# Optimization experiments

Measured on AMD Instinct MI355X. Metric: run time of the kernel, lower is better.

The kernel has to match this reference:

```python
import jax, jax.numpy as jnp
import numpy as np


def _conv2d(x, w, b):
    # 3x3 conv, stride 1, pad 1, NCHW
    y = jax.lax.conv_general_dilated(x, w, (1, 1), ((1, 1), (1, 1)),
                                     dimension_numbers=('NCHW', 'OIHW', 'NCHW'))
    return y + b[None, :, None, None]


def _up2(x):
    return jnp.repeat(jnp.repeat(x, 2, axis=2), 2, axis=3)


def _mdconv(x, w, b, ow, ob):
    # Modulated deformable conv v2 (mmcv semantics): 3x3, stride 1, pad 1,
    # dilation 1, deformable_groups=1. Offsets/mask predicted by conv_offset,
    # out = chunk3 -> (o1, o2, mask); offset = cat(o1, o2); mask = sigmoid(mask).
    B, Cin, H, W = x.shape
    off = _conv2d(x, ow, ob)                        # [B,27,H,W]
    o1, o2, m = jnp.split(off, 3, axis=1)
    offs = jnp.concatenate([o1, o2], axis=1)        # [B,18,H,W]
    dy, dx = offs[:, 0::2], offs[:, 1::2]           # [B,9,H,W] (dy,dx interleaved per kernel pt)
    mask = jax.nn.sigmoid(m)                        # [B,9,H,W]
    ky, kx = jnp.meshgrid(jnp.arange(3), jnp.arange(3), indexing='ij')
    # sampling positions: p0 + pn + offset (pad=1)
    py = jnp.arange(H, dtype=x.dtype)[None, None, :, None] - 1.0 + ky.reshape(1, 9, 1, 1) + dy
    px = jnp.arange(W, dtype=x.dtype)[None, None, None, :] - 1.0 + kx.reshape(1, 9, 1, 1) + dx
    y0 = jnp.floor(py); x0 = jnp.floor(px)
    wy1 = py - y0; wx1 = px - x0
    y0i = y0.astype(jnp.int32); x0i = x0.astype(jnp.int32)
    flat = x.reshape(B, Cin, H * W)

    def gather(yi, xi):
        valid = ((yi >= 0) & (yi < H) & (xi >= 0) & (xi < W)).astype(x.dtype)  # zero padding
        idx = jnp.clip(yi, 0, H - 1) * W + jnp.clip(xi, 0, W - 1)             # [B,9,H,W]
        g = jax.vmap(lambda f, i: f[:, i])(flat, idx)                          # [B,Cin,9,H,W]
        return g * valid[:, None]

    val = (gather(y0i, x0i) * ((1 - wy1) * (1 - wx1))[:, None]
           + gather(y0i, x0i + 1) * ((1 - wy1) * wx1)[:, None]
           + gather(y0i + 1, x0i) * (wy1 * (1 - wx1))[:, None]
           + gather(y0i + 1, x0i + 1) * (wy1 * wx1)[:, None])
    cols = val * mask[:, None]                      # [B,Cin,9,H,W]
    out = jnp.einsum('ock,bckhw->bohw', w.reshape(w.shape[0], Cin, 9), cols)
    return out + b[None, :, None, None]


def setup_inputs() -> dict:
    key = jax.random.key(0)
    ks = jax.random.split(key, 24)
    C = 256
    sizes = [(96, 96), (48, 48), (24, 24), (12, 12)]
    d = {}
    for i, (h, w) in enumerate(sizes):
        d[f'x{i}'] = jax.random.normal(ks[i], (2, C, h, w), dtype=jnp.float32)
    for i in range(4):
        d[f'w{i}'] = jax.random.normal(ks[4 + i], (C, C, 3, 3), dtype=jnp.float32) * 0.02
        d[f'b{i}'] = jax.random.normal(ks[8 + i], (C,), dtype=jnp.float32) * 0.02
    for i in range(1, 4):
        d[f'ow{i}'] = jax.random.normal(ks[12 + i], (27, C, 3, 3), dtype=jnp.float32) * 0.01
        d[f'ob{i}'] = jax.random.normal(ks[16 + i], (27,), dtype=jnp.float32) * 0.01
    return d


def reference(x0, x1, x2, x3, w0, w1, w2, w3, b0, b1, b2, b3,
              ow1, ow2, ow3, ob1, ob2, ob3):
    # tdm_convs[3] called with level=1 -> deform; the same-size nearest interpolate is identity
    t3 = _mdconv(x3, w3, b3, ow3, ob3)
    # i=3: tdm_convs[2](2, x2 + up(t3)) -> deform
    t2 = _mdconv(x2 + _up2(t3), w2, b2, ow2, ob2)
    # i=2: tdm_convs[1](1, x1 + up(t2)) -> deform
    t1 = _mdconv(x1 + _up2(t2), w1, b1, ow1, ob1)
    # i=1: tdm_convs[0](0, x0 + up(t1)) -> level 0 < start_level -> plain conv
    t0 = _conv2d(x0 + _up2(t1), w0, b0)
    return (t0, t1, t2, t3)
```

## Files before the change

### kernel.cpp

```cpp
#include <hip/hip_runtime.h>
#include <math.h>

__device__ __forceinline__ ushort f2bf(float f) {
    unsigned int u = __float_as_uint(f);
    u += 0x7FFFu + ((u >> 16) & 1u);
    return (ushort)(u >> 16);
}

typedef __attribute__((address_space(1))) const unsigned int guint;
typedef __attribute__((address_space(3))) unsigned int luint;
__device__ __forceinline__ void gload_lds16(const void* g, void* l) {
    __builtin_amdgcn_global_load_lds((guint*)g, (luint*)l, 16, 0, 0);
}

using bfrag = __attribute__((ext_vector_type(8))) short;
using f4    = __attribute__((ext_vector_type(4))) float;

__device__ __forceinline__ void bf8_to_f(uint4 v, float* o) {
    unsigned int u[4] = {v.x, v.y, v.z, v.w};
    #pragma unroll
    for (int i = 0; i < 4; ++i) {
        o[2 * i]     = __uint_as_float(u[i] << 16);
        o[2 * i + 1] = __uint_as_float(u[i] & 0xFFFF0000u);
    }
}

struct CvtArgs {
    const float* src[7];
    ushort*      dst[7];
    int          m[7];
};
__global__ __launch_bounds__(256) void cvt_kernel(CvtArgs a) {
    int t = blockIdx.y;
    int idx = blockIdx.x * 256 + threadIdx.x;
    int M = a.m[t];
    if (idx >= M * 288) return;
    int m = idx / 288, rem = idx - m * 288;
    int r = rem >> 5, c8 = rem & 31;
    const float* s = a.src[t] + ((size_t)(m * 256 + c8 * 8)) * 9 + r;
    ushort vals[8];
    #pragma unroll
    for (int j = 0; j < 8; ++j) vals[j] = f2bf(s[j * 9]);
    *(uint4*)&a.dst[t][(size_t)m * 2304 + r * 256 + c8 * 8] = *(uint4*)vals;
}

struct FillArgs {
    float* outp[3];
    const float* bias[3];
    int HW[3];
    float* zbase;
    int z4;
};
__global__ __launch_bounds__(256) void fill_kernel(FillArgs a) {
    int y = blockIdx.y;
    int i = blockIdx.x * 256 + threadIdx.x;
    if (y < 3) {
        int HW = a.HW[y];
        int total4 = (2 * 256 * HW) >> 2;
        if (i < total4) {
            int e = i << 2;
            int m = (e / HW) & 255;
            float v = a.bias[y][m];
            *(float4*)&a.outp[y][e] = float4{v, v, v, v};
        }
    } else {
        if (i < a.z4) ((float4*)a.zbase)[i] = float4{0.f, 0.f, 0.f, 0.f};
    }
}

__global__ __launch_bounds__(256) void xs_nhwc(
    const float* __restrict__ x, const float* __restrict__ prev,
    ushort* __restrict__ xs, int H, int W)
{
    __shared__ ushort tile[32][72];
    const int HW = H * W, W2 = W >> 1;
    int b = blockIdx.z, c0 = blockIdx.y * 32, hw0 = blockIdx.x * 64;
    const float* xb = x + ((size_t)b * 256 + c0) * HW;
    const float* pb = prev ? prev + ((size_t)b * 256 + c0) * (HW >> 2) : nullptr;

    int hwl = threadIdx.x & 63, cl0 = threadIdx.x >> 6;
    int hw = hw0 + hwl;
    bool ok = hw < HW;
    int hwc = ok ? hw : HW - 1;
    int h = hwc / W, w = hwc - h * W;
    int pidx = (h >> 1) * W2 + (w >> 1);
    #pragma unroll
    for (int p = 0; p < 8; ++p) {
        int cl = p * 4 + cl0;
        float v = 0.f;
        if (ok) {
            v = xb[(size_t)cl * HW + hw];
            if (pb) v += pb[(size_t)cl * (HW >> 2) + pidx];
        }
        tile[cl][hwl] = f2bf(v);
    }
    __syncthreads();
    int hwl2 = threadIdx.x >> 2, cc = (threadIdx.x & 3) * 8;
    int hw2 = hw0 + hwl2;
    if (hw2 < HW) {
        ushort vals[8];
        #pragma unroll
        for (int j = 0; j < 8; ++j) vals[j] = tile[cc + j][hwl2];
        *(uint4*)&xs[((size_t)b * HW + hw2) * 256 + c0 + cc] = *(uint4*)vals;
    }
}

__global__ __launch_bounds__(256) void off_mfma(
    const ushort* __restrict__ A, const ushort* __restrict__ xs,
    const ushort* __restrict__ zeros, float* __restrict__ offbuf,
    int N, int H, int W, int ktiles)
{
    __shared__ __align__(16) ushort As[2][32 * 32];
    __shared__ __align__(16) ushort Bs[2][64 * 32];
    const int b  = blockIdx.z;
    const int n0 = blockIdx.x * 64;
    const int kt0 = blockIdx.y * ktiles * 32;
    const int tid = threadIdx.x, lane = tid & 63, wv = tid >> 6;
    const ushort* xb = xs + (size_t)b * N * 256;

    int n = n0 + (tid >> 2); if (n >= N) n = N - 1;
    int h = n / W, w = n - h * W;
    int kcc = (tid & 3) * 8;

    auto stage = [&](int kt, int bi) {
        int r = kt >> 8, c0k = kt & 255;
        int ry = r / 3 - 1, rx = r - (r / 3) * 3 - 1;
        if (tid < 128) {
            int row = tid >> 2; if (row > 26) row = 26;
            gload_lds16(A + (size_t)row * 2304 + kt + kcc,
                        (char*)As[bi] + (size_t)(tid & ~63) * 16);
        }
        int ih = h + ry, iw = w + rx;
        const ushort* src = (ih >= 0 && ih < H && iw >= 0 && iw < W)
            ? xb + (((size_t)(ih * W + iw)) << 8) + c0k + kcc
            : zeros;
        gload_lds16(src, (char*)Bs[bi] + (size_t)(tid & ~63) * 16);
    };

    f4 acc[2] = {};
    stage(kt0, 0);
    for (int kk = 0; kk < ktiles; ++kk) {
        __syncthreads();
        if (kk + 1 < ktiles) stage(kt0 + (kk + 1) * 32, (kk + 1) & 1);
        const ushort* as = As[kk & 1];
        const ushort* bs = Bs[kk & 1];
        bfrag bf = *(const bfrag*)&bs[(wv * 16 + (lane & 15)) * 32 + (lane >> 4) * 8];
        bfrag a0 = *(const bfrag*)&as[(lane & 15) * 32 + (lane >> 4) * 8];
        bfrag a1 = *(const bfrag*)&as[(16 + (lane & 15)) * 32 + (lane >> 4) * 8];
        acc[0] = __builtin_amdgcn_mfma_f32_16x16x32_bf16(a0, bf, acc[0], 0, 0, 0);
        acc[1] = __builtin_amdgcn_mfma_f32_16x16x32_bf16(a1, bf, acc[1], 0, 0, 0);
    }

    int nn = n0 + wv * 16 + (lane & 15);
    if (nn < N) {
        #pragma unroll
        for (int mb = 0; mb < 2; ++mb)
            #pragma unroll
            for (int t = 0; t < 4; ++t) {
                int m = mb * 16 + (lane >> 4) * 4 + t;
                if (m < 27)
                    atomicAdd(&offbuf[((size_t)b * 27 + m) * N + nn], acc[mb][t]);
            }
    }
}

__global__ __launch_bounds__(256) void sampling_kernel(
    const ushort* __restrict__ xs, const float* __restrict__ off,
    const float* __restrict__ ob, ushort* __restrict__ cols,
    int H, int W)
{
    __shared__ float4 gw[32][9];
    __shared__ int4   go[32][9];
    const int HW = H * W;
    const int b = blockIdx.z;
    const int hw0 = blockIdx.x * 32;
    const int tid = threadIdx.x;
    const float* offb = off + (size_t)b * 27 * HW;
    const ushort* xb = xs + (size_t)b * HW * 256;

    for (int it = tid; it < 32 * 9; it += 256) {
        int hwl = it / 9, k = it - hwl * 9;
        int hw = hw0 + hwl; if (hw >= HW) hw = HW - 1;
        int h = hw / W, w = hw - h * W;
        float dy = offb[(size_t)(2 * k) * HW + hw] + ob[2 * k];
        float dx = offb[(size_t)(2 * k + 1) * HW + hw] + ob[2 * k + 1];
        float mv = offb[(size_t)(18 + k) * HW + hw] + ob[18 + k];
        float mk = 1.0f / (1.0f + __expf(-mv));
        float py = (float)h - 1.0f + (float)(k / 3) + dy;
        float px = (float)w - 1.0f + (float)(k % 3) + dx;
        float y0f = floorf(py), x0f = floorf(px);
        float wy = py - y0f, wx = px - x0f;
        int y0 = (int)y0f, x0i = (int)x0f;
        int y1 = y0 + 1, x1 = x0i + 1;
        bool vy0 = (y0 >= 0) & (y0 < H), vy1 = (y1 >= 0) & (y1 < H);
        bool vx0 = (x0i >= 0) & (x0i < W), vx1 = (x1 >= 0) & (x1 < W);
        float w00 = (1.f - wy) * (1.f - wx) * ((vy0 & vx0) ? mk : 0.f);
        float w01 = (1.f - wy) * wx        * ((vy0 & vx1) ? mk : 0.f);
        float w10 = wy * (1.f - wx)        * ((vy1 & vx0) ? mk : 0.f);
        float w11 = wy * wx                * ((vy1 & vx1) ? mk : 0.f);
        int cy0 = min(max(y0, 0), H - 1), cy1 = min(max(y1, 0), H - 1);
        int cx0 = min(max(x0i, 0), W - 1), cx1 = min(max(x1, 0), W - 1);
        gw[hwl][k] = float4{w00, w01, w10, w11};
        go[hwl][k] = int4{(cy0 * W + cx0) << 8, (cy0 * W + cx1) << 8,
                          (cy1 * W + cx0) << 8, (cy1 * W + cx1) << 8};
    }
    __syncthreads();

    int hwl = tid >> 3, cb = (tid & 7) * 32;
    int hw = hw0 + hwl;
    if (hw >= HW) return;
    ushort* colp = cols + ((size_t)b * HW + hw) * 2304 + cb;

    #pragma unroll
    for (int k = 0; k < 9; ++k) {
        float4 wv = gw[hwl][k];
        int4   ov = go[hwl][k];
        const ushort* p00 = xb + ov.x + cb;
        const ushort* p01 = xb + ov.y + cb;
        const ushort* p10 = xb + ov.z + cb;
        const ushort* p11 = xb + ov.w + cb;
        #pragma unroll
        for (int j = 0; j < 4; ++j) {
            float f00[8], f01[8], f10[8], f11[8];
            bf8_to_f(*(const uint4*)(p00 + 8 * j), f00);
            bf8_to_f(*(const uint4*)(p01 + 8 * j), f01);
            bf8_to_f(*(const uint4*)(p10 + 8 * j), f10);
            bf8_to_f(*(const uint4*)(p11 + 8 * j), f11);
            unsigned int pk[4];
            #pragma unroll
            for (int t = 0; t < 4; ++t) {
                float lo = f00[2 * t] * wv.x + f01[2 * t] * wv.y +
                           f10[2 * t] * wv.z + f11[2 * t] * wv.w;
                float hi = f00[2 * t + 1] * wv.x + f01[2 * t + 1] * wv.y +
                           f10[2 * t + 1] * wv.z + f11[2 * t + 1] * wv.w;
                pk[t] = (unsigned int)f2bf(lo) | ((unsigned int)f2bf(hi) << 16);
            }
            *(uint4*)(colp + k * 256 + 8 * j) = make_uint4(pk[0], pk[1], pk[2], pk[3]);
        }
    }
}

template<bool IMPLICIT, bool SPLITK>
__global__ __launch_bounds__(256) void mfma_gemm(
    const ushort* __restrict__ A, const float* __restrict__ bias,
    const ushort* __restrict__ Bt, const ushort* __restrict__ zeros,
    float* __restrict__ outp, int N, int H, int W, int kchunk)
{
    __shared__ __align__(16) ushort As[2][64 * 64];
    __shared__ __align__(16) ushort Bs[2][64 * 64];
    const int b  = blockIdx.z;
    const int m0 = (blockIdx.y & 3) * 64;
    const int kt0 = (blockIdx.y >> 2) * kchunk;
    const int n0 = blockIdx.x * 64;
    const int tid  = threadIdx.x;
    const int lane = tid & 63;
    const int wv   = tid >> 6;
    const int wm = wv & 1, wn = wv >> 1;

    const ushort* Bb = IMPLICIT ? Bt + (size_t)b * N * 256
                                : Bt + (size_t)b * (size_t)N * 2304;

    const int sc8 = ((tid & 7) ^ ((tid >> 3) & 7)) * 8;
    const int srow = tid >> 3;
    int bn[2], bh[2], bw[2];
    #pragma unroll
    for (int j = 0; j < 2; ++j) {
        int n = n0 + j * 32 + srow; if (n >= N) n = N - 1;
        bn[j] = n; bh[j] = n / W; bw[j] = n - bh[j] * W;
    }

    auto stage = [&](int kt, int bi) {
        #pragma unroll
        for (int i = 0; i < 2; ++i) {
            gload_lds16(A + (size_t)(m0 + i * 32 + srow) * 2304 + kt + sc8,
                        (char*)As[bi] + (size_t)(i * 256 + (tid & ~63)) * 16);
        }
        if (!IMPLICIT) {
            #pragma unroll
            for (int j = 0; j < 2; ++j)
                gload_lds16(Bb + (size_t)bn[j] * 2304 + kt + sc8,
                            (char*)Bs[bi] + (size_t)(j * 256 + (tid & ~63)) * 16);
        } else {
            int r = kt >> 8, c0k = kt & 255;
            int ry = r / 3 - 1, rx = r - (r / 3) * 3 - 1;
            #pragma unroll
            for (int j = 0; j < 2; ++j) {
                int ih = bh[j] + ry, iw = bw[j] + rx;
                const ushort* src = (ih >= 0 && ih < H && iw >= 0 && iw < W)
                    ? Bb + (((size_t)(ih * W + iw)) << 8) + c0k + sc8
                    : zeros;
                gload_lds16(src, (char*)Bs[bi] + (size_t)(j * 256 + (tid & ~63)) * 16);
            }
        }
    };

    const int fq = (lane >> 4);
    const int fv = (lane & 7);
    f4 acc[2][2] = {};

    const int nit = kchunk >> 6;
    stage(kt0, 0);
    for (int it = 0; it < nit; ++it) {
        __syncthreads();
        if (it + 1 < nit) stage(kt0 + (it + 1) * 64, (it + 1) & 1);
        const ushort* as = As[it & 1];
        const ushort* bs = Bs[it & 1];
        bfrag af[2][2], bf[2][2];
        #pragma unroll
        for (int kh = 0; kh < 2; ++kh) {
            int ch = ((kh * 4 + fq) ^ fv) * 8;
            #pragma unroll
            for (int i = 0; i < 2; ++i)
                af[kh][i] = *(const bfrag*)&as[(wm * 32 + i * 16 + (lane & 15)) * 64 + ch];
            #pragma unroll
            for (int j = 0; j < 2; ++j)
                bf[kh][j] = *(const bfrag*)&bs[(wn * 32 + j * 16 + (lane & 15)) * 64 + ch];
        }
        #pragma unroll
        for (int kh = 0; kh < 2; ++kh)
            #pragma unroll
            for (int i = 0; i < 2; ++i)
                #pragma unroll
                for (int j = 0; j < 2; ++j)
                    acc[i][j] = __builtin_amdgcn_mfma_f32_16x16x32_bf16(
                        af[kh][i], bf[kh][j], acc[i][j], 0, 0, 0);
    }

    const int mb = m0 + wm * 32, nb = n0 + wn * 32;
    #pragma unroll
    for (int i = 0; i < 2; ++i) {
        int mrow = mb + i * 16 + (lane >> 4) * 4;
        #pragma unroll
        for (int j = 0; j < 2; ++j) {
            int n = nb + j * 16 + (lane & 15);
            if (n < N) {
                #pragma unroll
                for (int t = 0; t < 4; ++t) {
                    int m = mrow + t;
                    if (SPLITK)
                        atomicAdd(&outp[((size_t)b * 256 + m) * N + n], acc[i][j][t]);
                    else
                        outp[((size_t)b * 256 + m) * N + n] = acc[i][j][t] + bias[m];
                }
            }
        }
    }
}

extern "C" void kernel_launch(void* const* d_in, const int* in_sizes, int n_in,
                              void* d_out, int out_size, void* d_ws, size_t ws_size,
                              hipStream_t stream)
{
    const float* x[4]   = {(const float*)d_in[0], (const float*)d_in[1],
                           (const float*)d_in[2], (const float*)d_in[3]};
    const float* wgt[4] = {(const float*)d_in[4], (const float*)d_in[6],
                           (const float*)d_in[8], (const float*)d_in[10]};
    const float* bia[4] = {(const float*)d_in[5], (const float*)d_in[7],
                           (const float*)d_in[9], (const float*)d_in[11]};
    const float* owt[4] = {nullptr, (const float*)d_in[12],
                           (const float*)d_in[14], (const float*)d_in[16]};
    const float* obv[4] = {nullptr, (const float*)d_in[13],
                           (const float*)d_in[15], (const float*)d_in[17]};

    const int B = 2;
    const int Hs[4] = {96, 48, 24, 12};
    const int HWs[4] = {96 * 96, 48 * 48, 24 * 24, 12 * 12};

    float* out = (float*)d_out;
    size_t outOff[4];
    outOff[0] = 0;
    outOff[1] = outOff[0] + (size_t)B * 256 * HWs[0];
    outOff[2] = outOff[1] + (size_t)B * 256 * HWs[1];
    outOff[3] = outOff[2] + (size_t)B * 256 * HWs[2];

    char* ws = (char*)d_ws;
    size_t off = 0;
    auto carve = [&](size_t bytes) { void* p = ws + off; off = (off + bytes + 255) & ~(size_t)255; return p; };
    ushort* wbf[4];
    ushort* owbf[4] = {nullptr, nullptr, nullptr, nullptr};
    for (int i = 0; i < 4; ++i) wbf[i] = (ushort*)carve((size_t)256 * 2304 * 2);
    for (int i = 1; i < 4; ++i) owbf[i] = (ushort*)carve((size_t)27 * 2304 * 2);
    ushort* cols = (ushort*)carve((size_t)B * HWs[1] * 2304 * 2);
    ushort* xsb[4];
    for (int i = 0; i < 4; ++i) xsb[i] = (ushort*)carve((size_t)B * 256 * HWs[i] * 2);
    int offElems = B * 27 * (HWs[1] + HWs[2] + HWs[3]);
    float* offbase = (float*)carve((size_t)offElems * 4 + 1024);
    ushort* zeros = (ushort*)(offbase + offElems);
    float* offbuf[4] = {nullptr,
                        offbase,
                        offbase + (size_t)B * 27 * HWs[1],
                        offbase + (size_t)B * 27 * (HWs[1] + HWs[2])};

    {
        CvtArgs a;
        a.src[0] = wgt[0]; a.src[1] = wgt[1]; a.src[2] = wgt[2]; a.src[3] = wgt[3];
        a.src[4] = owt[1]; a.src[5] = owt[2]; a.src[6] = owt[3];
        a.dst[0] = wbf[0]; a.dst[1] = wbf[1]; a.dst[2] = wbf[2]; a.dst[3] = wbf[3];
        a.dst[4] = owbf[1]; a.dst[5] = owbf[2]; a.dst[6] = owbf[3];
        for (int i = 0; i < 4; ++i) a.m[i] = 256;
        for (int i = 4; i < 7; ++i) a.m[i] = 27;
        dim3 grd((256 * 288 + 255) / 256, 7);
        cvt_kernel<<<grd, 256, 0, stream>>>(a);
    }
    {
        FillArgs a;
        for (int i = 0; i < 3; ++i) {
            a.outp[i] = out + outOff[i + 1]; a.bias[i] = bia[i + 1]; a.HW[i] = HWs[i + 1];
        }
        a.zbase = offbase;
        a.z4 = (offElems * 4 + 1024) / 16;
        int maxE = 2 * 256 * HWs[1] / 4;
        if (a.z4 > maxE) maxE = a.z4;
        dim3 grd((maxE + 255) / 256, 4);
        fill_kernel<<<grd, 256, 0, stream>>>(a);
    }
    {
        dim3 grd((HWs[3] + 63) / 64, 8, B);
        xs_nhwc<<<grd, 256, 0, stream>>>(x[3], nullptr, xsb[3], Hs[3], Hs[3]);
    }

    const int ktiles[4] = {0, 9, 6, 3};
    const int ksplit[4] = {1, 2, 4, 6};

    for (int lvl = 3; lvl >= 1; --lvl) {
        int H = Hs[lvl], W = H, HW = HWs[lvl];

        {
            dim3 grd((HW + 63) / 64, 72 / ktiles[lvl], B);
            off_mfma<<<grd, 256, 0, stream>>>(
                owbf[lvl], xsb[lvl], zeros, offbuf[lvl], HW, H, W, ktiles[lvl]);
        }
        {
            dim3 grd((HW + 31) / 32, 1, B);
            sampling_kernel<<<grd, 256, 0, stream>>>(
                xsb[lvl], offbuf[lvl], obv[lvl], cols, H, W);
        }
        {
            dim3 grd((HW + 63) / 64, 4 * ksplit[lvl], B);
            mfma_gemm<false, true><<<grd, 256, 0, stream>>>(
                wbf[lvl], bia[lvl], cols, zeros, out + outOff[lvl],
                HW, H, W, 2304 / ksplit[lvl]);
        }
        {
            int Hn = Hs[lvl - 1];
            dim3 grd((HWs[lvl - 1] + 63) / 64, 8, B);
            xs_nhwc<<<grd, 256, 0, stream>>>(
                x[lvl - 1], out + outOff[lvl], xsb[lvl - 1], Hn, Hn);
        }
    }

    {
        dim3 grd((HWs[0] + 63) / 64, 4, B);
        mfma_gemm<true, false><<<grd, 256, 0, stream>>>(
            wbf[0], bia[0], xsb[0], zeros, out + outOff[0],
            HWs[0], Hs[0], Hs[0], 2304);
    }
}
```

Before: 297.0 us.

## Fuse prologue kernels into one launch and widen GEMM M tile to 128

Merges the weight conversion, bias/zero fill and first NHWC transpose into a single prolog kernel, so two kernel launches are gone. The MFMA GEMM tile grows from 64 to 128 output channels per block, which gives each wave four M sub-tiles and more reuse of each B tile. Split-K factors for the smaller levels are raised to make up for the halved grid. The cost is more LDS and registers per block, fewer blocks for the final plain conv, and more atomic traffic at the small levels.

```diff
diff --git a/kernel.cpp b/kernel.cpp
--- a/kernel.cpp
+++ b/kernel.cpp
@@ -25,56 +25,13 @@
     }
 }
 
-struct CvtArgs {
-    const float* src[7];
-    ushort*      dst[7];
-    int          m[7];
-};
-__global__ __launch_bounds__(256) void cvt_kernel(CvtArgs a) {
-    int t = blockIdx.y;
-    int idx = blockIdx.x * 256 + threadIdx.x;
-    int M = a.m[t];
-    if (idx >= M * 288) return;
-    int m = idx / 288, rem = idx - m * 288;
-    int r = rem >> 5, c8 = rem & 31;
-    const float* s = a.src[t] + ((size_t)(m * 256 + c8 * 8)) * 9 + r;
-    ushort vals[8];
-    #pragma unroll
-    for (int j = 0; j < 8; ++j) vals[j] = f2bf(s[j * 9]);
-    *(uint4*)&a.dst[t][(size_t)m * 2304 + r * 256 + c8 * 8] = *(uint4*)vals;
-}
-
-struct FillArgs {
-    float* outp[3];
-    const float* bias[3];
-    int HW[3];
-    float* zbase;
-    int z4;
-};
-__global__ __launch_bounds__(256) void fill_kernel(FillArgs a) {
-    int y = blockIdx.y;
-    int i = blockIdx.x * 256 + threadIdx.x;
-    if (y < 3) {
-        int HW = a.HW[y];
-        int total4 = (2 * 256 * HW) >> 2;
-        if (i < total4) {
-            int e = i << 2;
-            int m = (e / HW) & 255;
-            float v = a.bias[y][m];
-            *(float4*)&a.outp[y][e] = float4{v, v, v, v};
-        }
-    } else {
-        if (i < a.z4) ((float4*)a.zbase)[i] = float4{0.f, 0.f, 0.f, 0.f};
-    }
-}
-
-__global__ __launch_bounds__(256) void xs_nhwc(
+__device__ __forceinline__ void xs_body(void* smem,
     const float* __restrict__ x, const float* __restrict__ prev,
-    ushort* __restrict__ xs, int H, int W)
-{
-    __shared__ ushort tile[32][72];
+    ushort* __restrict__ xs, int H, int W, int bx, int by, int bz)
+{
+    ushort (*tile)[72] = (ushort(*)[72])smem;
     const int HW = H * W, W2 = W >> 1;
-    int b = blockIdx.z, c0 = blockIdx.y * 32, hw0 = blockIdx.x * 64;
+    int b = bz, c0 = by * 32, hw0 = bx * 64;
     const float* xb = x + ((size_t)b * 256 + c0) * HW;
     const float* pb = prev ? prev + ((size_t)b * 256 + c0) * (HW >> 2) : nullptr;
 
@@ -103,6 +60,60 @@
         for (int j = 0; j < 8; ++j) vals[j] = tile[cc + j][hwl2];
         *(uint4*)&xs[((size_t)b * HW + hw2) * 256 + c0 + cc] = *(uint4*)vals;
     }
+}
+
+struct ProArgs {
+    const float* wsrc[7];
+    ushort*      wdst[7];
+    float*       outp[3];
+    const float* bias[3];
+    int          HW[3];
+    float*       zbase;
+    int          z4;
+    const float* x3;
+    ushort*      xs3;
+};
+__global__ __launch_bounds__(256) void prolog_kernel(ProArgs a) {
+    __shared__ __align__(16) char smem[32 * 72 * 2];
+    int y = blockIdx.y;
+    if (y < 7) {
+        int M = (y < 4) ? 256 : 27;
+        int idx = blockIdx.x * 256 + threadIdx.x;
+        if (idx < M * 288) {
+            int m = idx / 288, rem = idx - m * 288;
+            int r = rem >> 5, c8 = rem & 31;
+            const float* s = a.wsrc[y] + ((size_t)(m * 256 + c8 * 8)) * 9 + r;
+            ushort vals[8];
+            #pragma unroll
+            for (int j = 0; j < 8; ++j) vals[j] = f2bf(s[j * 9]);
+            *(uint4*)&a.wdst[y][(size_t)m * 2304 + r * 256 + c8 * 8] = *(uint4*)vals;
+        }
+    } else if (y < 10) {
+        int t = y - 7;
+        int HW = a.HW[t];
+        int i = blockIdx.x * 256 + threadIdx.x;
+        if (i < 128 * HW) {
+            int e = i << 2;
+            int m = (e / HW) & 255;
+            float v = a.bias[t][m];
+            *(float4*)&a.outp[t][e] = float4{v, v, v, v};
+        }
+    } else if (y == 10) {
+        int i = blockIdx.x * 256 + threadIdx.x;
+        if (i < a.z4) ((float4*)a.zbase)[i] = float4{0.f, 0.f, 0.f, 0.f};
+    } else {
+        int vb = blockIdx.x;
+        if (vb < 48)
+            xs_body(smem, a.x3, nullptr, a.xs3, 12, 12, vb % 3, (vb / 3) & 7, vb / 24);
+    }
+}
+
+__global__ __launch_bounds__(256) void xs_nhwc(
+    const float* __restrict__ x, const float* __restrict__ prev,
+    ushort* __restrict__ xs, int H, int W)
+{
+    __shared__ __align__(16) char smem[32 * 72 * 2];
+    xs_body(smem, x, prev, xs, H, W, blockIdx.x, blockIdx.y, blockIdx.z);
 }
 
 __global__ __launch_bounds__(256) void off_mfma(
@@ -246,11 +257,11 @@
     const ushort* __restrict__ Bt, const ushort* __restrict__ zeros,
     float* __restrict__ outp, int N, int H, int W, int kchunk)
 {
-    __shared__ __align__(16) ushort As[2][64 * 64];
+    __shared__ __align__(16) ushort As[2][128 * 64];
     __shared__ __align__(16) ushort Bs[2][64 * 64];
     const int b  = blockIdx.z;
-    const int m0 = (blockIdx.y & 3) * 64;
-    const int kt0 = (blockIdx.y >> 2) * kchunk;
+    const int m0 = (blockIdx.y & 1) * 128;
+    const int kt0 = (blockIdx.y >> 1) * kchunk;
     const int n0 = blockIdx.x * 64;
     const int tid  = threadIdx.x;
     const int lane = tid & 63;
@@ -271,7 +282,7 @@
 
     auto stage = [&](int kt, int bi) {
         #pragma unroll
-        for (int i = 0; i < 2; ++i) {
+        for (int i = 0; i < 4; ++i) {
             gload_lds16(A + (size_t)(m0 + i * 32 + srow) * 2304 + kt + sc8,
                         (char*)As[bi] + (size_t)(i * 256 + (tid & ~63)) * 16);
         }
@@ -296,7 +307,7 @@
 
     const int fq = (lane >> 4);
     const int fv = (lane & 7);
-    f4 acc[2][2] = {};
+    f4 acc[4][2] = {};
 
     const int nit = kchunk >> 6;
     stage(kt0, 0);
@@ -305,13 +316,13 @@
         if (it + 1 < nit) stage(kt0 + (it + 1) * 64, (it + 1) & 1);
         const ushort* as = As[it & 1];
         const ushort* bs = Bs[it & 1];
-        bfrag af[2][2], bf[2][2];
+        bfrag af[2][4], bf[2][2];
         #pragma unroll
         for (int kh = 0; kh < 2; ++kh) {
             int ch = ((kh * 4 + fq) ^ fv) * 8;
             #pragma unroll
-            for (int i = 0; i < 2; ++i)
-                af[kh][i] = *(const bfrag*)&as[(wm * 32 + i * 16 + (lane & 15)) * 64 + ch];
+            for (int i = 0; i < 4; ++i)
+                af[kh][i] = *(const bfrag*)&as[(wm * 64 + i * 16 + (lane & 15)) * 64 + ch];
             #pragma unroll
             for (int j = 0; j < 2; ++j)
                 bf[kh][j] = *(const bfrag*)&bs[(wn * 32 + j * 16 + (lane & 15)) * 64 + ch];
@@ -319,16 +330,16 @@
         #pragma unroll
         for (int kh = 0; kh < 2; ++kh)
             #pragma unroll
-            for (int i = 0; i < 2; ++i)
+            for (int i = 0; i < 4; ++i)
                 #pragma unroll
                 for (int j = 0; j < 2; ++j)
                     acc[i][j] = __builtin_amdgcn_mfma_f32_16x16x32_bf16(
                         af[kh][i], bf[kh][j], acc[i][j], 0, 0, 0);
     }
 
-    const int mb = m0 + wm * 32, nb = n0 + wn * 32;
+    const int mb = m0 + wm * 64, nb = n0 + wn * 32;
     #pragma unroll
-    for (int i = 0; i < 2; ++i) {
+    for (int i = 0; i < 4; ++i) {
         int mrow = mb + i * 16 + (lane >> 4) * 4;
         #pragma unroll
         for (int j = 0; j < 2; ++j) {
@@ -392,35 +403,24 @@
                         offbase + (size_t)B * 27 * (HWs[1] + HWs[2])};
 
     {
-        CvtArgs a;
-        a.src[0] = wgt[0]; a.src[1] = wgt[1]; a.src[2] = wgt[2]; a.src[3] = wgt[3];
-        a.src[4] = owt[1]; a.src[5] = owt[2]; a.src[6] = owt[3];
-        a.dst[0] = wbf[0]; a.dst[1] = wbf[1]; a.dst[2] = wbf[2]; a.dst[3] = wbf[3];
-        a.dst[4] = owbf[1]; a.dst[5] = owbf[2]; a.dst[6] = owbf[3];
-        for (int i = 0; i < 4; ++i) a.m[i] = 256;
-        for (int i = 4; i < 7; ++i) a.m[i] = 27;
-        dim3 grd((256 * 288 + 255) / 256, 7);
-        cvt_kernel<<<grd, 256, 0, stream>>>(a);
-    }
-    {
-        FillArgs a;
+        ProArgs a;
+        a.wsrc[0] = wgt[0]; a.wsrc[1] = wgt[1]; a.wsrc[2] = wgt[2]; a.wsrc[3] = wgt[3];
+        a.wsrc[4] = owt[1]; a.wsrc[5] = owt[2]; a.wsrc[6] = owt[3];
+        a.wdst[0] = wbf[0]; a.wdst[1] = wbf[1]; a.wdst[2] = wbf[2]; a.wdst[3] = wbf[3];
+        a.wdst[4] = owbf[1]; a.wdst[5] = owbf[2]; a.wdst[6] = owbf[3];
         for (int i = 0; i < 3; ++i) {
             a.outp[i] = out + outOff[i + 1]; a.bias[i] = bia[i + 1]; a.HW[i] = HWs[i + 1];
         }
         a.zbase = offbase;
         a.z4 = (offElems * 4 + 1024) / 16;
-        int maxE = 2 * 256 * HWs[1] / 4;
-        if (a.z4 > maxE) maxE = a.z4;
-        dim3 grd((maxE + 255) / 256, 4);
-        fill_kernel<<<grd, 256, 0, stream>>>(a);
-    }
-    {
-        dim3 grd((HWs[3] + 63) / 64, 8, B);
-        xs_nhwc<<<grd, 256, 0, stream>>>(x[3], nullptr, xsb[3], Hs[3], Hs[3]);
+        a.x3 = x[3];
+        a.xs3 = xsb[3];
+        dim3 grd(1152, 12);
+        prolog_kernel<<<grd, 256, 0, stream>>>(a);
     }
 
     const int ktiles[4] = {0, 9, 6, 3};
-    const int ksplit[4] = {1, 2, 4, 6};
+    const int ksplit[4] = {1, 2, 6, 12};
 
     for (int lvl = 3; lvl >= 1; --lvl) {
         int H = Hs[lvl], W = H, HW = HWs[lvl];
@@ -436,7 +436,7 @@
                 xsb[lvl], offbuf[lvl], obv[lvl], cols, H, W);
         }
         {
-            dim3 grd((HW + 63) / 64, 4 * ksplit[lvl], B);
+            dim3 grd((HW + 63) / 64, 2 * ksplit[lvl], B);
             mfma_gemm<false, true><<<grd, 256, 0, stream>>>(
                 wbf[lvl], bia[lvl], cols, zeros, out + outOff[lvl],
                 HW, H, W, 2304 / ksplit[lvl]);
@@ -450,7 +450,7 @@
     }
 
     {
-        dim3 grd((HWs[0] + 63) / 64, 4, B);
+        dim3 grd((HWs[0] + 63) / 64, 2, B);
         mfma_gemm<true, false><<<grd, 256, 0, stream>>>(
             wbf[0], bia[0], xsb[0], zeros, out + outOff[0],
             HWs[0], Hs[0], Hs[0], 2304);
```

Measured after the change: 286.0 us. 1.04x faster.
